# Optimization experiments

Hardware: AMD Instinct MI355X
Metric: run time of the kernel (lower is better)

Reference implementation:

```python
import jax, jax.numpy as jnp
import numpy as np
from jax import lax

EPS = 1e-10
DELU_P = 10.0

def delu(x):
    # delu_feature_map: param*relu(x) + (exp(param*min(x,0)) - 1) + 1
    x1 = jax.nn.relu(x)
    x2 = jnp.exp(DELU_P * (x - x1)) - 1.0
    return DELU_P * x1 + x2 + 1.0

def conv1x1(x, w, b):
    # x: (B,C,H,W), w: (O,C), b: (O,)
    return jnp.einsum('bchw,oc->bohw', x, w) + b[None, :, None, None]

def conv3x3(x, w, b):
    # w: (O,I,3,3), SAME padding, stride 1
    y = lax.conv_general_dilated(x, w, window_strides=(1, 1), padding='SAME',
                                 dimension_numbers=('NCHW', 'OIHW', 'NCHW'))
    return y + b[None, :, None, None]

def setup_inputs() -> dict:
    key = jax.random.key(0)
    ks = jax.random.split(key, 12)
    B, C, H, W = 4, 256, 128, 128
    s = 0.02
    return {
        'x':   jax.random.normal(ks[0], (B, C, H, W), dtype=jnp.float32),
        'wq':  jax.random.normal(ks[1], (C, C), dtype=jnp.float32) * s,
        'bq':  jax.random.normal(ks[2], (C,), dtype=jnp.float32) * s,
        'wk':  jax.random.normal(ks[3], (C, C), dtype=jnp.float32) * s,
        'bk':  jax.random.normal(ks[4], (C,), dtype=jnp.float32) * s,
        'wv':  jax.random.normal(ks[5], (C, C), dtype=jnp.float32) * s,
        'bv':  jax.random.normal(ks[6], (C,), dtype=jnp.float32) * s,
        'wd1': jax.random.normal(ks[7], (C, C), dtype=jnp.float32) * s,
        'bd1': jax.random.normal(ks[8], (C,), dtype=jnp.float32) * s,
        'wd3': jax.random.normal(ks[9], (C, C, 3, 3), dtype=jnp.float32) * s,
        'bd3': jax.random.normal(ks[10], (C,), dtype=jnp.float32) * s,
        'gamma': jax.random.normal(ks[11], (1,), dtype=jnp.float32) * 0.1,
    }

def reference(x, wq, bq, wk, bk, wv, bv, wd1, bd1, wd3, bd3, gamma):
    B, C, H, W = x.shape
    N = H * W
    # q/k/v projections flattened to (B, C, N)
    q = conv1x1(x, wq, bq).reshape(B, C, N)
    k = conv1x1(x, wk, bk).reshape(B, C, N)
    v = conv1x1(x, wv, bv).reshape(B, C, N)
    # feature maps (torch permutes q to (B,N,C), applies map, permutes back -> elementwise, no-op layout)
    q = delu(q)
    k = delu(k)
    # energy: (B, C, C), contracting over spatial N (q indexed 'bmn')
    energy = jnp.einsum('bmn,bcn->bmc', q, k)
    KV = k * v  # (B, C, N) elementwise
    norm = 1.0 / (jnp.einsum('bmc,bcn->bn', energy, k) + EPS)  # (B, N)
    # attention: sum over m of energy, times KV, times norm -> (B, C, N)
    attention = jnp.einsum('bmc,bcn,bn->bcn', energy, KV, norm)
    out = attention.reshape(B, C, H, W)
    out = out + conv1x1(x, wd1, bd1) + conv3x3(x, wd3, bd3)
    return x + gamma[0] * out
```

## Files before the change

### kernel.cpp

```cpp
#include <hip/hip_runtime.h>

#define BB 4
#define CC 256
#define HH 128
#define WW 128
#define NN (HH*WW)
#define EPSF 1e-10f

#define XR 130
#define XPB ((size_t)XR*XR*CC)

typedef __bf16 bf16x8 __attribute__((ext_vector_type(8)));
typedef float  f32x4  __attribute__((ext_vector_type(4)));
typedef float  f32x16 __attribute__((ext_vector_type(16)));

__device__ __forceinline__ float delu_f(float v) {
    return v > 0.0f ? fmaf(10.0f, v, 1.0f) : __expf(10.0f * v);
}

__device__ __forceinline__ void gl_lds16(const __bf16* g, __bf16* l) {
    __builtin_amdgcn_global_load_lds(
        (const __attribute__((address_space(1))) void*)g,
        (__attribute__((address_space(3))) void*)l, 16, 0, 0);
}

__global__ __launch_bounds__(256) void k_prep(const float* __restrict__ wq,
    const float* __restrict__ wk, const float* __restrict__ wv,
    const float* __restrict__ wd1, const float* __restrict__ wd3,
    __bf16* __restrict__ wqb, __bf16* __restrict__ wkb, __bf16* __restrict__ wvb,
    __bf16* __restrict__ wcv32)
{
    int idx = blockIdx.x * 256 + threadIdx.x;
    if (idx >= CC*CC) return;
    const int oc = idx >> 8, ic = idx & 255;
    const int kb = ic >> 5, ocf = oc >> 4;
    const int lane = ((ic >> 3) & 3)*16 + (oc & 15);
    const int e = ic & 7;
    const size_t off = ((size_t)(kb*16 + ocf)*64 + lane)*8 + e;
    wqb[off] = (__bf16)wq[idx];
    wkb[off] = (__bf16)wk[idx];
    wvb[off] = (__bf16)wv[idx];
    const int ocf32 = oc >> 5;
    const int gks = ic >> 4, khi = (ic >> 3) & 1;
    const int lane32 = khi*32 + (oc & 31);
    const size_t off32 = ((size_t)((gks*8 + ocf32))*64 + lane32)*8 + e;
    float w9[9];
    #pragma unroll
    for (int k=0;k<9;k++) w9[k] = wd3[(size_t)idx*9 + k];
    w9[4] += wd1[idx];
    #pragma unroll
    for (int t=0;t<9;t++) wcv32[(size_t)t*CC*CC + off32] = (__bf16)w9[t];
}

__global__ __launch_bounds__(256) void k_xpad(const float* __restrict__ x,
                                              __bf16* __restrict__ xpad)
{
    const int xrow = blockIdx.x;
    const int b    = blockIdx.y;
    const int tid  = threadIdx.x;
    const int hr   = xrow - 1;
    const float* xb = x + (size_t)b*CC*NN;
    __bf16* xpb = xpad + (size_t)b*XPB + (size_t)xrow*XR*CC;
    const bool rowok = (hr >= 0 && hr < HH);
    for (int t = tid; t < XR*32; t += 256) {
        int xcol = t % XR, icg = t / XR;
        int wc = xcol - 1;
        bf16x8 v8 = {};
        if (rowok && wc >= 0 && wc < WW) {
            const float* p = xb + (size_t)(icg*8)*NN + hr*WW + wc;
            #pragma unroll
            for (int j=0;j<8;j++) v8[j] = (__bf16)p[(size_t)j*NN];
        }
        *(bf16x8*)&xpb[(size_t)xcol*CC + icg*8] = v8;
    }
}

__device__ __forceinline__ void stage_tile_async(const __bf16* __restrict__ xrb,
                                                 __bf16* __restrict__ xs,
                                                 int wid, int lane)
{
    #pragma unroll
    for (int j = 0; j < 8; ++j) {
        const int kq = wid + 4*j;
        gl_lds16(xrb + (size_t)lane*CC + kq*8, &xs[(size_t)kq*64*8]);
    }
}

__device__ __forceinline__ void mfma_gemm_l(const __bf16* __restrict__ wb,
                                            const __bf16* __restrict__ xs,
                                            int ocf0, int lane, int l15, int lq,
                                            f32x4 acc[4][4])
{
    #pragma unroll
    for (int kb=0; kb<8; kb++) {
        bf16x8 af[4], bfr[4];
        #pragma unroll
        for (int f=0; f<4; f++)
            af[f] = *(const bf16x8*)&wb[(size_t)((kb*16 + ocf0 + f)*64 + lane)*8];
        #pragma unroll
        for (int nf=0; nf<4; nf++)
            bfr[nf] = *(const bf16x8*)&xs[(size_t)((kb*4 + lq)*64 + nf*16 + l15)*8];
        #pragma unroll
        for (int f=0; f<4; f++)
            #pragma unroll
            for (int nf=0; nf<4; nf++)
                acc[f][nf] = __builtin_amdgcn_mfma_f32_16x16x32_bf16(af[f], bfr[nf], acc[f][nf], 0, 0, 0);
    }
}

__global__ __launch_bounds__(256) void k_qk_mfma(const __bf16* __restrict__ xpad,
    const __bf16* __restrict__ wqb, const float* __restrict__ bq,
    const __bf16* __restrict__ wkb, const float* __restrict__ bk,
    __bf16* __restrict__ kp, float* __restrict__ Qs)
{
    __shared__ __bf16 xs[32*64*8];
    __shared__ float Qpart[4][64];
    const int n0 = blockIdx.x * 64;
    const int b  = blockIdx.y;
    const int tid = threadIdx.x;
    const int wid = tid >> 6, lane = tid & 63;
    const int l15 = lane & 15, lq = lane >> 4;
    const int oc_base = wid*64;
    const int h = n0 >> 7, w0 = n0 & 127;
    const __bf16* xrb = xpad + (size_t)b*XPB + ((size_t)(h+1)*XR + w0 + 1)*CC;

    stage_tile_async(xrb, xs, wid, lane);
    __syncthreads();

    f32x4 acc[4][4] = {};
    mfma_gemm_l(wqb, xs, wid*4, lane, l15, lq, acc);
    #pragma unroll
    for (int nf=0; nf<4; nf++) {
        float s = 0.0f;
        #pragma unroll
        for (int f=0; f<4; f++)
            #pragma unroll
            for (int r=0; r<4; r++)
                s += delu_f(acc[f][nf][r] + bq[oc_base + f*16 + lq*4 + r]);
        s += __shfl_xor(s, 16);
        s += __shfl_xor(s, 32);
        if (lq == 0) Qpart[wid][nf*16 + l15] = s;
    }
    __syncthreads();
    if (tid < 64)
        Qs[(size_t)b*NN + n0 + tid] = Qpart[0][tid] + Qpart[1][tid] + Qpart[2][tid] + Qpart[3][tid];

    #pragma unroll
    for (int f=0; f<4; f++)
        #pragma unroll
        for (int nf=0; nf<4; nf++)
            acc[f][nf] = (f32x4){0.f,0.f,0.f,0.f};
    mfma_gemm_l(wkb, xs, wid*4, lane, l15, lq, acc);
    #pragma unroll
    for (int f=0; f<4; f++) {
        #pragma unroll
        for (int r=0; r<4; r++) {
            const int oc = oc_base + f*16 + lq*4 + r;
            const float bias = bk[oc];
            __bf16* kr = kp + ((size_t)b*CC + oc)*NN + n0;
            #pragma unroll
            for (int nf=0; nf<4; nf++)
                kr[nf*16 + l15] = (__bf16)delu_f(acc[f][nf][r] + bias);
        }
    }
}

__global__ __launch_bounds__(256) void k_esum(const __bf16* __restrict__ kp,
    const float* __restrict__ Qs, float* __restrict__ Es)
{
    const int c = blockIdx.x & (CC-1), b = blockIdx.x >> 8;
    const int tid = threadIdx.x;
    const bf16x8* kr = (const bf16x8*)(kp + ((size_t)b*CC + c)*NN);
    const float4* qr = (const float4*)(Qs + (size_t)b*NN);
    float s = 0.0f;
    for (int i = tid; i < NN/8; i += 256) {
        bf16x8 kk = kr[i];
        float4 q0 = qr[2*i], q1 = qr[2*i+1];
        s += (float)kk[0]*q0.x + (float)kk[1]*q0.y + (float)kk[2]*q0.z + (float)kk[3]*q0.w
           + (float)kk[4]*q1.x + (float)kk[5]*q1.y + (float)kk[6]*q1.z + (float)kk[7]*q1.w;
    }
    #pragma unroll
    for (int m=1; m<64; m<<=1) s += __shfl_xor(s, m, 64);
    __shared__ float red[4];
    if ((tid & 63) == 0) red[tid >> 6] = s;
    __syncthreads();
    if (tid == 0) Es[b*CC + c] = red[0] + red[1] + red[2] + red[3];
}

__global__ __launch_bounds__(256) void k_vattn_mfma(const float* __restrict__ x,
    const __bf16* __restrict__ xpad,
    const __bf16* __restrict__ wvb, const float* __restrict__ bv,
    const __bf16* __restrict__ kp, const float* __restrict__ Es,
    const float* __restrict__ gamma, float* __restrict__ out)
{
    __shared__ __bf16 xs[32*64*8];
    __shared__ float Dpart[4][64];
    __shared__ float rn_sh[64];
    const int n0 = blockIdx.x * 64;
    const int b  = blockIdx.y;
    const int tid = threadIdx.x;
    const int wid = tid >> 6, lane = tid & 63;
    const int l15 = lane & 15, lq = lane >> 4;
    const int oc_base = wid*64;
    const int h = n0 >> 7, w0 = n0 & 127;
    const __bf16* xrb = xpad + (size_t)b*XPB + ((size_t)(h+1)*XR + w0 + 1)*CC;

    stage_tile_async(xrb, xs, wid, lane);
    __syncthreads();

    f32x4 acc[4][4] = {};
    mfma_gemm_l(wvb, xs, wid*4, lane, l15, lq, acc);

    float dpart[4] = {0.f,0.f,0.f,0.f};
    #pragma unroll
    for (int f=0; f<4; f++) {
        #pragma unroll
        for (int r=0; r<4; r++) {
            const int oc = oc_base + f*16 + lq*4 + r;
            const float e = Es[b*CC + oc];
            const __bf16* kr = kp + ((size_t)b*CC + oc)*NN + n0;
            #pragma unroll
            for (int nf=0; nf<4; nf++)
                dpart[nf] = fmaf(e, (float)kr[nf*16 + l15], dpart[nf]);
        }
    }
    #pragma unroll
    for (int nf=0; nf<4; nf++) {
        dpart[nf] += __shfl_xor(dpart[nf], 16);
        dpart[nf] += __shfl_xor(dpart[nf], 32);
        if (lq == 0) Dpart[wid][nf*16 + l15] = dpart[nf];
    }
    __syncthreads();
    if (tid < 64)
        rn_sh[tid] = 1.0f / (Dpart[0][tid] + Dpart[1][tid] + Dpart[2][tid] + Dpart[3][tid] + EPSF);
    __syncthreads();

    const float g = gamma[0];
    float rv[4];
    #pragma unroll
    for (int nf=0; nf<4; nf++) rv[nf] = rn_sh[nf*16 + l15];
    #pragma unroll
    for (int f=0; f<4; f++) {
        #pragma unroll
        for (int r=0; r<4; r++) {
            const int oc = oc_base + f*16 + lq*4 + r;
            const float eg = Es[b*CC + oc] * g;
            const float bias = bv[oc];
            const __bf16* kr = kp + ((size_t)b*CC + oc)*NN + n0;
            const float* xr  = x  + ((size_t)b*CC + oc)*NN + n0;
            float* orow = out + ((size_t)b*CC + oc)*NN + n0;
            #pragma unroll
            for (int nf=0; nf<4; nf++) {
                const int w = nf*16 + l15;
                orow[w] = fmaf(eg*(float)kr[w]*rv[nf], acc[f][nf][r] + bias, xr[w]);
            }
        }
    }
}

__global__ __launch_bounds__(256,2) void k_conv_mfma(const __bf16* __restrict__ xpad,
    const __bf16* __restrict__ wcv32, const float* __restrict__ bd1,
    const float* __restrict__ bd3, const float* __restrict__ gamma,
    float* __restrict__ out)
{
    __shared__ __bf16 xs[2][12*132*8];
    const int orig = blockIdx.x;
    const int wg   = (orig & 7)*64 + (orig >> 3);
    const int b    = wg >> 7;
    const int h    = wg & 127;
    const int tid = threadIdx.x;
    const int wid = tid >> 6, lane = tid & 63;
    const int l31 = lane & 31, lhi = lane >> 5;
    const int oc_base = wid*64;
    const __bf16* xpb = xpad + (size_t)b*XPB;

    f32x16 acc[2][4] = {};

    #define STAGE_CV(bufsel, icb) do {                                          \
        const int ic0_ = (icb)*32;                                              \
        _Pragma("unroll")                                                       \
        for (int j = 0; j < 9; ++j) {                                           \
            const int w_ = wid + 4*j;                                           \
            const int pair_ = w_ / 3, chunk_ = w_ % 3;                          \
            const int r_ = pair_ >> 2, icq_ = pair_ & 3;                        \
            const int col0_ = chunk_ * 64;                                      \
            if (col0_ + lane < XR)                                              \
                gl_lds16(xpb + ((size_t)(h + r_)*XR + col0_ + lane)*CC + ic0_ + icq_*8, \
                         &xs[bufsel][(size_t)(pair_*132 + col0_)*8]);           \
        }                                                                       \
    } while (0)

    #define AF_LOAD(dst, t, icb)                                                \
        _Pragma("unroll")                                                       \
        for (int f=0; f<2; f++)                                                 \
            _Pragma("unroll")                                                   \
            for (int kk=0; kk<2; kk++)                                          \
                dst[f*2+kk] = *(const bf16x8*)&wcv32[((size_t)(t)*CC*CC) +      \
                    ((size_t)((((icb)*2 + kk)*8 + wid*2 + f))*64 + lane)*8];

    STAGE_CV(0, 0);
    __syncthreads();

    #pragma unroll 1
    for (int icb = 0; icb < 8; ++icb) {
        const __bf16* xb = xs[icb & 1];
        bf16x8 af2[2][4];
        AF_LOAD(af2[0], 0, icb);
        if (icb < 7) STAGE_CV((icb+1)&1, icb+1);
        #pragma unroll
        for (int t=0; t<9; ++t) {
            const int cur = t & 1, nxt = cur ^ 1;
            const int ky = t/3, kx = t%3;
            if (t < 8) { AF_LOAD(af2[nxt], t+1, icb); }
            __builtin_amdgcn_s_setprio(1);
            #pragma unroll
            for (int kk=0; kk<2; kk++) {
                #pragma unroll
                for (int nf=0; nf<4; nf++) {
                    bf16x8 br = *(const bf16x8*)&xs[icb & 1][
                        (size_t)((ky*4 + kk*2 + lhi)*132 + nf*32 + l31 + kx)*8];
                    #pragma unroll
                    for (int f=0; f<2; f++)
                        acc[f][nf] = __builtin_amdgcn_mfma_f32_32x32x16_bf16(
                            af2[cur][f*2+kk], br, acc[f][nf], 0, 0, 0);
                }
            }
            __builtin_amdgcn_s_setprio(0);
        }
        __syncthreads();
    }
    #undef STAGE_CV
    #undef AF_LOAD

    const float g = gamma[0];
    #pragma unroll
    for (int f=0; f<2; f++) {
        #pragma unroll
        for (int reg=0; reg<16; reg++) {
            const int row = (reg & 3) + 8*(reg >> 2) + 4*lhi;
            const int oc = oc_base + f*32 + row;
            const float bias = bd1[oc] + bd3[oc];
            float* orow = out + ((size_t)b*CC + oc)*NN + (size_t)h*WW;
            #pragma unroll
            for (int nf=0; nf<4; nf++) {
                const int w = nf*32 + l31;
                orow[w] += g*(acc[f][nf][reg] + bias);
            }
        }
    }
}

extern "C" void kernel_launch(void* const* d_in, const int* in_sizes, int n_in,
                              void* d_out, int out_size, void* d_ws, size_t ws_size,
                              hipStream_t stream)
{
    const float* x     = (const float*)d_in[0];
    const float* wq    = (const float*)d_in[1];
    const float* bq    = (const float*)d_in[2];
    const float* wk    = (const float*)d_in[3];
    const float* bk    = (const float*)d_in[4];
    const float* wv    = (const float*)d_in[5];
    const float* bv    = (const float*)d_in[6];
    const float* wd1   = (const float*)d_in[7];
    const float* bd1   = (const float*)d_in[8];
    const float* wd3   = (const float*)d_in[9];
    const float* bd3   = (const float*)d_in[10];
    const float* gamma = (const float*)d_in[11];
    float* out = (float*)d_out;

    __bf16* kp    = (__bf16*)d_ws;
    float*  Qs    = (float*)(kp + (size_t)BB*CC*NN);
    float*  Es    = Qs + (size_t)BB*NN;
    __bf16* wcv32 = (__bf16*)(Es + (size_t)BB*CC);
    __bf16* wqb   = wcv32 + (size_t)9*CC*CC;
    __bf16* wkb   = wqb + (size_t)CC*CC;
    __bf16* wvb   = wkb + (size_t)CC*CC;
    __bf16* xpad  = wvb + (size_t)CC*CC;

    k_prep      <<<dim3(CC*CC/256), 256, 0, stream>>>(wq, wk, wv, wd1, wd3, wqb, wkb, wvb, wcv32);
    k_xpad      <<<dim3(XR, BB), 256, 0, stream>>>(x, xpad);
    k_qk_mfma   <<<dim3(NN/64, BB), 256, 0, stream>>>(xpad, wqb, bq, wkb, bk, kp, Qs);
    k_esum      <<<dim3(BB*CC), 256, 0, stream>>>(kp, Qs, Es);
    k_vattn_mfma<<<dim3(NN/64, BB), 256, 0, stream>>>(x, xpad, wvb, bv, kp, Es, gamma, out);
    k_conv_mfma <<<dim3(HH*BB), 256, 0, stream>>>(xpad, wcv32, bd1, bd3, gamma, out);
}
```

Measured before the change: 190.8 us.

## Switch QK and V projection kernels to 32x32 MFMA over full 128-pixel rows

The q/k and v projection kernels now process a whole image row (128 pixels) per block instead of 64 pixels, and use 32x32x16 bf16 MFMA instead of 16x16x32. The projection weights are repacked into the same 32-wide fragment layout the conv kernel already uses, and LDS staging gets a padded 132-stride layout. The aim is to halve weight-fragment reloads per pixel and raise MFMA efficiency, at the cost of launching half as many blocks (512 each) and higher register use in the epilogue.

```diff
diff --git a/kernel.cpp b/kernel.cpp
--- a/kernel.cpp
+++ b/kernel.cpp
@@ -33,17 +33,14 @@
     int idx = blockIdx.x * 256 + threadIdx.x;
     if (idx >= CC*CC) return;
     const int oc = idx >> 8, ic = idx & 255;
-    const int kb = ic >> 5, ocf = oc >> 4;
-    const int lane = ((ic >> 3) & 3)*16 + (oc & 15);
-    const int e = ic & 7;
-    const size_t off = ((size_t)(kb*16 + ocf)*64 + lane)*8 + e;
-    wqb[off] = (__bf16)wq[idx];
-    wkb[off] = (__bf16)wk[idx];
-    wvb[off] = (__bf16)wv[idx];
     const int ocf32 = oc >> 5;
     const int gks = ic >> 4, khi = (ic >> 3) & 1;
     const int lane32 = khi*32 + (oc & 31);
-    const size_t off32 = ((size_t)((gks*8 + ocf32))*64 + lane32)*8 + e;
+    const int e = ic & 7;
+    const size_t off32 = ((size_t)(gks*8 + ocf32)*64 + lane32)*8 + e;
+    wqb[off32] = (__bf16)wq[idx];
+    wkb[off32] = (__bf16)wk[idx];
+    wvb[off32] = (__bf16)wv[idx];
     float w9[9];
     #pragma unroll
     for (int k=0;k<9;k++) w9[k] = wd3[(size_t)idx*9 + k];
@@ -75,36 +72,40 @@
     }
 }
 
-__device__ __forceinline__ void stage_tile_async(const __bf16* __restrict__ xrb,
-                                                 __bf16* __restrict__ xs,
-                                                 int wid, int lane)
-{
-    #pragma unroll
-    for (int j = 0; j < 8; ++j) {
-        const int kq = wid + 4*j;
-        gl_lds16(xrb + (size_t)lane*CC + kq*8, &xs[(size_t)kq*64*8]);
-    }
-}
-
-__device__ __forceinline__ void mfma_gemm_l(const __bf16* __restrict__ wb,
+__device__ __forceinline__ void stage_row128(const __bf16* __restrict__ xrb,
+                                             __bf16* __restrict__ xs,
+                                             int wid, int lane)
+{
+    #pragma unroll
+    for (int j = 0; j < 16; ++j) {
+        const int it = wid + 4*j;
+        const int kq = it >> 1, ch = it & 1;
+        gl_lds16(xrb + (size_t)(ch*64 + lane)*CC + kq*8, &xs[(size_t)(kq*132 + ch*64)*8]);
+    }
+}
+
+__device__ __forceinline__ void mfma_gemm32(const __bf16* __restrict__ wb,
                                             const __bf16* __restrict__ xs,
-                                            int ocf0, int lane, int l15, int lq,
-                                            f32x4 acc[4][4])
+                                            int wid, int lane, int l31, int lhi,
+                                            f32x16 acc[2][4])
 {
     #pragma unroll
     for (int kb=0; kb<8; kb++) {
-        bf16x8 af[4], bfr[4];
-        #pragma unroll
-        for (int f=0; f<4; f++)
-            af[f] = *(const bf16x8*)&wb[(size_t)((kb*16 + ocf0 + f)*64 + lane)*8];
-        #pragma unroll
-        for (int nf=0; nf<4; nf++)
-            bfr[nf] = *(const bf16x8*)&xs[(size_t)((kb*4 + lq)*64 + nf*16 + l15)*8];
-        #pragma unroll
-        for (int f=0; f<4; f++)
-            #pragma unroll
-            for (int nf=0; nf<4; nf++)
-                acc[f][nf] = __builtin_amdgcn_mfma_f32_16x16x32_bf16(af[f], bfr[nf], acc[f][nf], 0, 0, 0);
+        bf16x8 af[4];
+        #pragma unroll
+        for (int f=0; f<2; f++)
+            #pragma unroll
+            for (int kk=0; kk<2; kk++)
+                af[f*2+kk] = *(const bf16x8*)&wb[((size_t)((kb*2+kk)*8 + wid*2 + f)*64 + lane)*8];
+        #pragma unroll
+        for (int kk=0; kk<2; kk++)
+            #pragma unroll
+            for (int nf=0; nf<4; nf++) {
+                bf16x8 br = *(const bf16x8*)&xs[(size_t)((kb*4 + kk*2 + lhi)*132 + nf*32 + l31)*8];
+                #pragma unroll
+                for (int f=0; f<2; f++)
+                    acc[f][nf] = __builtin_amdgcn_mfma_f32_32x32x16_bf16(af[f*2+kk], br, acc[f][nf], 0, 0, 0);
+            }
     }
 }
 
@@ -113,54 +114,55 @@
     const __bf16* __restrict__ wkb, const float* __restrict__ bk,
     __bf16* __restrict__ kp, float* __restrict__ Qs)
 {
-    __shared__ __bf16 xs[32*64*8];
-    __shared__ float Qpart[4][64];
-    const int n0 = blockIdx.x * 64;
+    __shared__ __bf16 xs[32*132*8];
+    __shared__ float Qpart[4][128];
+    const int h  = blockIdx.x;
+    const int n0 = h * 128;
     const int b  = blockIdx.y;
     const int tid = threadIdx.x;
     const int wid = tid >> 6, lane = tid & 63;
-    const int l15 = lane & 15, lq = lane >> 4;
+    const int l31 = lane & 31, lhi = lane >> 5;
     const int oc_base = wid*64;
-    const int h = n0 >> 7, w0 = n0 & 127;
-    const __bf16* xrb = xpad + (size_t)b*XPB + ((size_t)(h+1)*XR + w0 + 1)*CC;
-
-    stage_tile_async(xrb, xs, wid, lane);
-    __syncthreads();
-
-    f32x4 acc[4][4] = {};
-    mfma_gemm_l(wqb, xs, wid*4, lane, l15, lq, acc);
+    const __bf16* xrb = xpad + (size_t)b*XPB + ((size_t)(h+1)*XR + 1)*CC;
+
+    stage_row128(xrb, xs, wid, lane);
+    __syncthreads();
+
+    f32x16 acc[2][4] = {};
+    mfma_gemm32(wqb, xs, wid, lane, l31, lhi, acc);
     #pragma unroll
     for (int nf=0; nf<4; nf++) {
         float s = 0.0f;
         #pragma unroll
-        for (int f=0; f<4; f++)
-            #pragma unroll
-            for (int r=0; r<4; r++)
-                s += delu_f(acc[f][nf][r] + bq[oc_base + f*16 + lq*4 + r]);
-        s += __shfl_xor(s, 16);
+        for (int f=0; f<2; f++)
+            #pragma unroll
+            for (int reg=0; reg<16; reg++) {
+                const int oc = oc_base + f*32 + (reg&3) + 8*(reg>>2) + 4*lhi;
+                s += delu_f(acc[f][nf][reg] + bq[oc]);
+            }
         s += __shfl_xor(s, 32);
-        if (lq == 0) Qpart[wid][nf*16 + l15] = s;
-    }
-    __syncthreads();
-    if (tid < 64)
+        if (lhi == 0) Qpart[wid][nf*32 + l31] = s;
+    }
+    __syncthreads();
+    if (tid < 128)
         Qs[(size_t)b*NN + n0 + tid] = Qpart[0][tid] + Qpart[1][tid] + Qpart[2][tid] + Qpart[3][tid];
 
     #pragma unroll
-    for (int f=0; f<4; f++)
+    for (int f=0; f<2; f++)
         #pragma unroll
         for (int nf=0; nf<4; nf++)
-            acc[f][nf] = (f32x4){0.f,0.f,0.f,0.f};
-    mfma_gemm_l(wkb, xs, wid*4, lane, l15, lq, acc);
-    #pragma unroll
-    for (int f=0; f<4; f++) {
-        #pragma unroll
-        for (int r=0; r<4; r++) {
-            const int oc = oc_base + f*16 + lq*4 + r;
+            acc[f][nf] = (f32x16){};
+    mfma_gemm32(wkb, xs, wid, lane, l31, lhi, acc);
+    #pragma unroll
+    for (int f=0; f<2; f++) {
+        #pragma unroll
+        for (int reg=0; reg<16; reg++) {
+            const int oc = oc_base + f*32 + (reg&3) + 8*(reg>>2) + 4*lhi;
             const float bias = bk[oc];
             __bf16* kr = kp + ((size_t)b*CC + oc)*NN + n0;
             #pragma unroll
             for (int nf=0; nf<4; nf++)
-                kr[nf*16 + l15] = (__bf16)delu_f(acc[f][nf][r] + bias);
+                kr[nf*32 + l31] = (__bf16)delu_f(acc[f][nf][reg] + bias);
         }
     }
 }
@@ -193,57 +195,53 @@
     const __bf16* __restrict__ kp, const float* __restrict__ Es,
     const float* __restrict__ gamma, float* __restrict__ out)
 {
-    __shared__ __bf16 xs[32*64*8];
-    __shared__ float Dpart[4][64];
-    __shared__ float rn_sh[64];
-    const int n0 = blockIdx.x * 64;
+    __shared__ __bf16 xs[32*132*8];
+    __shared__ float Dpart[4][128];
+    __shared__ float rn_sh[128];
+    const int h  = blockIdx.x;
+    const int n0 = h * 128;
     const int b  = blockIdx.y;
     const int tid = threadIdx.x;
     const int wid = tid >> 6, lane = tid & 63;
-    const int l15 = lane & 15, lq = lane >> 4;
+    const int l31 = lane & 31, lhi = lane >> 5;
     const int oc_base = wid*64;
-    const int h = n0 >> 7, w0 = n0 & 127;
-    const __bf16* xrb = xpad + (size_t)b*XPB + ((size_t)(h+1)*XR + w0 + 1)*CC;
-
-    stage_tile_async(xrb, xs, wid, lane);
-    __syncthreads();
-
-    f32x4 acc[4][4] = {};
-    mfma_gemm_l(wvb, xs, wid*4, lane, l15, lq, acc);
+    const __bf16* xrb = xpad + (size_t)b*XPB + ((size_t)(h+1)*XR + 1)*CC;
+
+    stage_row128(xrb, xs, wid, lane);
+    __syncthreads();
+
+    f32x16 acc[2][4] = {};
+    mfma_gemm32(wvb, xs, wid, lane, l31, lhi, acc);
 
     float dpart[4] = {0.f,0.f,0.f,0.f};
     #pragma unroll
-    for (int f=0; f<4; f++) {
-        #pragma unroll
-        for (int r=0; r<4; r++) {
-            const int oc = oc_base + f*16 + lq*4 + r;
+    for (int f=0; f<2; f++) {
+        #pragma unroll
+        for (int reg=0; reg<16; reg++) {
+            const int oc = oc_base + f*32 + (reg&3) + 8*(reg>>2) + 4*lhi;
             const float e = Es[b*CC + oc];
             const __bf16* kr = kp + ((size_t)b*CC + oc)*NN + n0;
             #pragma unroll
             for (int nf=0; nf<4; nf++)
-                dpart[nf] = fmaf(e, (float)kr[nf*16 + l15], dpart[nf]);
+                dpart[nf] = fmaf(e, (float)kr[nf*32 + l31], dpart[nf]);
         }
     }
     #pragma unroll
     for (int nf=0; nf<4; nf++) {
-        dpart[nf] += __shfl_xor(dpart[nf], 16);
         dpart[nf] += __shfl_xor(dpart[nf], 32);
-        if (lq == 0) Dpart[wid][nf*16 + l15] = dpart[nf];
-    }
-    __syncthreads();
-    if (tid < 64)
+        if (lhi == 0) Dpart[wid][nf*32 + l31] = dpart[nf];
+    }
+    __syncthreads();
+    if (tid < 128)
         rn_sh[tid] = 1.0f / (Dpart[0][tid] + Dpart[1][tid] + Dpart[2][tid] + Dpart[3][tid] + EPSF);
     __syncthreads();
 
     const float g = gamma[0];
-    float rv[4];
-    #pragma unroll
-    for (int nf=0; nf<4; nf++) rv[nf] = rn_sh[nf*16 + l15];
-    #pragma unroll
-    for (int f=0; f<4; f++) {
-        #pragma unroll
-        for (int r=0; r<4; r++) {
-            const int oc = oc_base + f*16 + lq*4 + r;
+    #pragma unroll
+    for (int f=0; f<2; f++) {
+        #pragma unroll
+        for (int reg=0; reg<16; reg++) {
+            const int oc = oc_base + f*32 + (reg&3) + 8*(reg>>2) + 4*lhi;
             const float eg = Es[b*CC + oc] * g;
             const float bias = bv[oc];
             const __bf16* kr = kp + ((size_t)b*CC + oc)*NN + n0;
@@ -251,8 +249,8 @@
             float* orow = out + ((size_t)b*CC + oc)*NN + n0;
             #pragma unroll
             for (int nf=0; nf<4; nf++) {
-                const int w = nf*16 + l15;
-                orow[w] = fmaf(eg*(float)kr[w]*rv[nf], acc[f][nf][r] + bias, xr[w]);
+                const int w = nf*32 + l31;
+                orow[w] = fmaf(eg*(float)kr[w]*rn_sh[w], acc[f][nf][reg] + bias, xr[w]);
             }
         }
     }
@@ -303,7 +301,6 @@
 
     #pragma unroll 1
     for (int icb = 0; icb < 8; ++icb) {
-        const __bf16* xb = xs[icb & 1];
         bf16x8 af2[2][4];
         AF_LOAD(af2[0], 0, icb);
         if (icb < 7) STAGE_CV((icb+1)&1, icb+1);
@@ -379,8 +376,8 @@
 
     k_prep      <<<dim3(CC*CC/256), 256, 0, stream>>>(wq, wk, wv, wd1, wd3, wqb, wkb, wvb, wcv32);
     k_xpad      <<<dim3(XR, BB), 256, 0, stream>>>(x, xpad);
-    k_qk_mfma   <<<dim3(NN/64, BB), 256, 0, stream>>>(xpad, wqb, bq, wkb, bk, kp, Qs);
+    k_qk_mfma   <<<dim3(HH, BB), 256, 0, stream>>>(xpad, wqb, bq, wkb, bk, kp, Qs);
     k_esum      <<<dim3(BB*CC), 256, 0, stream>>>(kp, Qs, Es);
-    k_vattn_mfma<<<dim3(NN/64, BB), 256, 0, stream>>>(x, xpad, wvb, bv, kp, Es, gamma, out);
+    k_vattn_mfma<<<dim3(HH, BB), 256, 0, stream>>>(x, xpad, wvb, bv, kp, Es, gamma, out);
     k_conv_mfma <<<dim3(HH*BB), 256, 0, stream>>>(xpad, wcv32, bd1, bd3, gamma, out);
 }
```

Result: no change. 194.6 us (+2.0%).
